# Performance work log

Hardware: AMD Instinct MI355X
Metric: run time of the kernel (lower is better)

The kernel has to match this reference:

```python
import jax, jax.numpy as jnp
import numpy as np

N = 1024          # number of graph nodes
HIDDEN = 128
NUM_HEADS = 8
HEAD_DIM = HIDDEN // NUM_HEADS
E = 16384         # number of edges (avg degree 16)


def _linear_params(key, fin, fout):
    kw, _ = jax.random.split(key)
    W = jax.random.normal(kw, (fin, fout), jnp.float32) / np.sqrt(fin).astype(np.float32)
    b = jnp.zeros((fout,), jnp.float32)
    return W, b


def setup_inputs() -> dict:
    key = jax.random.key(0)
    ks = jax.random.split(key, 12)
    h_prev = jax.random.normal(ks[0], (N, HIDDEN), jnp.float32)
    h_pred = jax.random.normal(ks[1], (N, HIDDEN), jnp.float32)
    adj_rows = jax.random.randint(ks[2], (E,), 0, N, jnp.int32)
    adj_cols = jax.random.randint(ks[3], (E,), 0, N, jnp.int32)
    Wq, bq = _linear_params(ks[4], HIDDEN, HIDDEN)
    Wk, bk = _linear_params(ks[5], HIDDEN, HIDDEN)
    Wv, bv = _linear_params(ks[6], HIDDEN, HIDDEN)
    Wo, bo = _linear_params(ks[7], HIDDEN, HIDDEN)
    gW1, gb1 = _linear_params(ks[8], 2 * HIDDEN, HIDDEN)   # gate MLP layer 1 (silu)
    gW2, gb2 = _linear_params(ks[9], HIDDEN, HIDDEN)       # gate MLP layer 2
    mW1, mb1 = _linear_params(ks[10], 2 * HIDDEN, HIDDEN)  # mixer MLP layer 1 (relu)
    mW2, mb2 = _linear_params(ks[11], HIDDEN, HIDDEN)      # mixer MLP layer 2
    return dict(h_prev=h_prev, h_pred=h_pred, adj_rows=adj_rows, adj_cols=adj_cols,
                Wq=Wq, bq=bq, Wk=Wk, bk=bk, Wv=Wv, bv=bv, Wo=Wo, bo=bo,
                gW1=gW1, gb1=gb1, gW2=gW2, gb2=gb2,
                mW1=mW1, mb1=mb1, mW2=mW2, mb2=mb2)


def reference(h_prev, h_pred, adj_rows, adj_cols,
              Wq, bq, Wk, bk, Wv, bv, Wo, bo,
              gW1, gb1, gW2, gb2, mW1, mb1, mW2, mb2):
    n = h_prev.shape[0]
    # projections, reshaped (n, head_dim, num_heads) exactly as in the source
    q = (h_pred @ Wq + bq).reshape(n, HEAD_DIM, NUM_HEADS)
    k = (h_prev @ Wk + bk).reshape(n, HEAD_DIM, NUM_HEADS)
    v = (h_pred @ Wv + bv).reshape(n, HEAD_DIM, NUM_HEADS)
    # source scales by sqrt(k.shape[-1]) == sqrt(num_heads)
    q = q / jnp.sqrt(jnp.asarray(NUM_HEADS, q.dtype))
    # 'TNH,SNH->TNS': contracts over the num_heads axis -> [n, head_dim, n]
    scores = jnp.einsum('tnh,snh->tns', q, k)
    # bcoo_dot_general(adj, scores, (([1],[0]),([],[]))) == adj @ scores over node axis
    # (duplicate edges accumulate, matching BCOO semantics)
    A = jnp.zeros((n, n), scores.dtype).at[adj_rows, adj_cols].add(jnp.asarray(1.0, scores.dtype))
    attn = jnp.einsum('ts,snd->tnd', A, scores)   # [n, head_dim, n]
    attn = jax.nn.softmax(attn, axis=-1)
    # 'TNS,BNH->BNH': reduce attn over (T,S), broadcast onto v over head_dim axis
    y = jnp.einsum('TNS,BNH->BNH', attn, v)       # [n, head_dim, num_heads]
    out = y.reshape(n, HIDDEN) @ Wo + bo
    # gate MLP (2 layers, silu hidden act, no norm) then sigmoid
    cat = jnp.concatenate([h_pred, h_prev], axis=-1)
    gate = jax.nn.sigmoid(jax.nn.silu(cat @ gW1 + gb1) @ gW2 + gb2)
    out = gate * out
    h_corr = h_prev + out
    # mixer MLP (2 layers, relu hidden act, no norm), residual
    cat2 = jnp.concatenate([h_corr, h_prev], axis=-1)
    mixed = h_corr + (jax.nn.relu(cat2 @ mW1 + mb1) @ mW2 + mb2)
    return mixed
```

## Files before the change

kernel.cpp:

```cpp
#include <hip/hip_runtime.h>


#define HH 128
#define NROWS 1024
#define ROWS 4
#define NT 512
#define NG 16

#define WS_WV  0
#define WS_WO  8192
#define WS_GW1 16384
#define WS_GW2 32768
#define WS_MW1 40960
#define WS_MW2 57344

__device__ __forceinline__ unsigned int f2bf16(float f) {
    union { float f; unsigned int i; } x; x.f = f;
    unsigned int lsb = (x.i >> 16) & 1u;
    return (x.i + 0x7FFFu + lsb) >> 16;
}

__global__ __launch_bounds__(256) void convert_weights(
    const float* __restrict__ Wv,  const float* __restrict__ Wo,
    const float* __restrict__ gW1, const float* __restrict__ gW2,
    const float* __restrict__ mW1, const float* __restrict__ mW2,
    unsigned int* __restrict__ dst)
{
    const int b = blockIdx.x;
    const float* src; unsigned int* d; int lb;
    if      (b < 32)  { src = Wv;  d = dst + WS_WV;  lb = b; }
    else if (b < 64)  { src = Wo;  d = dst + WS_WO;  lb = b - 32; }
    else if (b < 128) { src = gW1; d = dst + WS_GW1; lb = b - 64; }
    else if (b < 160) { src = gW2; d = dst + WS_GW2; lb = b - 128; }
    else if (b < 224) { src = mW1; d = dst + WS_MW1; lb = b - 160; }
    else              { src = mW2; d = dst + WS_MW2; lb = b - 224; }
    const int e  = lb * 256 + threadIdx.x;
    const int k2 = e >> 7, j = e & 127;
    const unsigned int lo = f2bf16(src[(2 * k2) * HH + j]);
    const unsigned int hi = f2bf16(src[(2 * k2 + 1) * HH + j]);
    d[e] = lo | (hi << 16);
}

__device__ __forceinline__ void fma4(float4& a, float s, const float4& w) {
    a.x += s * w.x; a.y += s * w.y; a.z += s * w.z; a.w += s * w.w;
}
__device__ __forceinline__ float4 bflo4(uint4 q) {
    return make_float4(__uint_as_float(q.x << 16), __uint_as_float(q.y << 16),
                       __uint_as_float(q.z << 16), __uint_as_float(q.w << 16));
}
__device__ __forceinline__ float4 bfhi4(uint4 q) {
    return make_float4(__uint_as_float(q.x & 0xffff0000u), __uint_as_float(q.y & 0xffff0000u),
                       __uint_as_float(q.z & 0xffff0000u), __uint_as_float(q.w & 0xffff0000u));
}

__global__ __launch_bounds__(NT) void temporal_attn_fused(
    const float* __restrict__ h_prev,
    const float* __restrict__ h_pred,
    const unsigned int* __restrict__ wbf,
    const float* __restrict__ bv,  const float* __restrict__ bo,
    const float* __restrict__ gb1, const float* __restrict__ gb2,
    const float* __restrict__ mb1, const float* __restrict__ mb2,
    float* __restrict__ out)
{
    __shared__ __align__(16) float sPred[ROWS][HH];
    __shared__ __align__(16) float sPrev[ROWS][HH];
    __shared__ __align__(16) float sBuf[ROWS][HH];
    __shared__ __align__(16) float sCorr[ROWS][HH];
    __shared__ __align__(16) float sAtt[ROWS][HH];
    __shared__ float4 part4[NG][ROWS][HH / 4];

    const int tid = threadIdx.x;
    const int jq  = tid & 31;
    const int cg  = ((tid >> 5) + blockIdx.x) & 15;
    const int rr  = tid >> 7;
    const int jj  = tid & (HH - 1);
    const int r0  = blockIdx.x * ROWS;

    sPred[rr][jj] = h_pred[(r0 + rr) * HH + jj];
    sPrev[rr][jj] = h_prev[(r0 + rr) * HH + jj];
    const float rbv  = bv[jj],  rbo  = bo[jj];
    const float rgb1 = gb1[jj], rgb2 = gb2[jj];
    const float rmb1 = mb1[jj], rmb2 = mb2[jj];
    __syncthreads();

    const float* pf = (const float*)part4;
    const int cbase = rr * HH + jj;

    uint4 wa[8], wb[8];
    float4 acc[ROWS];

    #define LWB(dst, off, wsoff, rp) { \
        const uint4* B4 = (const uint4*)(wbf + (wsoff)); \
        _Pragma("unroll") for (int i = 0; i < 4; ++i) \
            dst[(off) + i] = B4[((rp) + 4 * cg + i) * 32 + jq]; }

    #define ZACC() { _Pragma("unroll") for (int r = 0; r < ROWS; ++r) \
        acc[r] = make_float4(0.f, 0.f, 0.f, 0.f); }

    #define FMAB(S, wp, woff) { \
        _Pragma("unroll") for (int i = 0; i < 4; ++i) { \
            float4 wl = bflo4(wp[(woff) + i]); \
            float4 wh = bfhi4(wp[(woff) + i]); \
            _Pragma("unroll") for (int r = 0; r < ROWS; ++r) { \
                fma4(acc[r], S[r][8 * cg + 2 * i],     wl); \
                fma4(acc[r], S[r][8 * cg + 2 * i + 1], wh); } } }

    #define PSTORE() { \
        _Pragma("unroll") for (int r = 0; r < ROWS; ++r) part4[cg][r][jq] = acc[r]; \
        __syncthreads(); }

    #define COMBINE(dotvar) \
        float dotvar = 0.f; \
        _Pragma("unroll") for (int g = 0; g < NG; ++g) dotvar += pf[g * (ROWS * HH) + cbase];

    LWB(wa, 0, WS_WV, 0);
    LWB(wb, 0, WS_WO, 0);
    ZACC(); FMAB(sPred, wa, 0);
    LWB(wa, 0, WS_GW1, 0);
    LWB(wa, 4, WS_GW1, 64);
    PSTORE();
    { COMBINE(dot); sBuf[rr][jj] = 1024.f * (dot + rbv); }
    __syncthreads();

    ZACC(); FMAB(sBuf, wb, 0);
    LWB(wb, 0, WS_GW2, 0);
    PSTORE();
    { COMBINE(dot); sAtt[rr][jj] = dot + rbo; }
    __syncthreads();

    ZACC(); FMAB(sPred, wa, 0); FMAB(sPrev, wa, 4);
    LWB(wa, 0, WS_MW1, 0);
    LWB(wa, 4, WS_MW1, 64);
    PSTORE();
    { COMBINE(dot);
      float x = dot + rgb1;
      sBuf[rr][jj] = x / (1.f + __expf(-x)); }
    __syncthreads();

    ZACC(); FMAB(sBuf, wb, 0);
    LWB(wb, 0, WS_MW2, 0);
    PSTORE();
    { COMBINE(dot);
      float gate = 1.f / (1.f + __expf(-(dot + rgb2)));
      sCorr[rr][jj] = sPrev[rr][jj] + gate * sAtt[rr][jj]; }
    __syncthreads();

    ZACC(); FMAB(sCorr, wa, 0); FMAB(sPrev, wa, 4);
    PSTORE();
    { COMBINE(dot); sBuf[rr][jj] = fmaxf(dot + rmb1, 0.f); }
    __syncthreads();

    ZACC(); FMAB(sBuf, wb, 0);
    PSTORE();
    { COMBINE(dot); out[(r0 + rr) * HH + jj] = sCorr[rr][jj] + dot + rmb2; }
}

extern "C" void kernel_launch(void* const* d_in, const int* in_sizes, int n_in,
                              void* d_out, int out_size, void* d_ws, size_t ws_size,
                              hipStream_t stream) {
    const float* h_prev = (const float*)d_in[0];
    const float* h_pred = (const float*)d_in[1];
    const float* Wv  = (const float*)d_in[8];
    const float* bv  = (const float*)d_in[9];
    const float* Wo  = (const float*)d_in[10];
    const float* bo  = (const float*)d_in[11];
    const float* gW1 = (const float*)d_in[12];
    const float* gb1 = (const float*)d_in[13];
    const float* gW2 = (const float*)d_in[14];
    const float* gb2 = (const float*)d_in[15];
    const float* mW1 = (const float*)d_in[16];
    const float* mb1 = (const float*)d_in[17];
    const float* mW2 = (const float*)d_in[18];
    const float* mb2 = (const float*)d_in[19];
    float* out = (float*)d_out;
    unsigned int* wbf = (unsigned int*)d_ws;

    hipLaunchKernelGGL(convert_weights, dim3(256), dim3(256), 0, stream,
                       Wv, Wo, gW1, gW2, mW1, mW2, wbf);

    hipLaunchKernelGGL(temporal_attn_fused, dim3(NROWS / ROWS), dim3(NT), 0, stream,
                       h_prev, h_pred, wbf, bv, bo, gb1, gb2, mb1, mb2, out);
}
```

Measured before the change: 99.70 us.

## Drop bf16 weight conversion kernel, read fp32 weights directly, process 8 rows per block

Removes the separate weight-conversion launch and reads the fp32 weights directly in the fused kernel, which also removes the bf16 unpacking. Each block now handles 8 rows instead of 4, halving the grid to 128 blocks so each weight load is reused across more rows. Shared-memory activations are read as float4 vectors. The cost is twice the weight bytes per block, higher register pressure (16+8 float4 weight registers plus 8 accumulators), and fewer blocks to fill the GPU.

After: 100.4 us. About the same (+0.7%).

```diff
diff --git a/kernel.cpp b/kernel.cpp
--- a/kernel.cpp
+++ b/kernel.cpp
@@ -3,63 +3,23 @@
 
 #define HH 128
 #define NROWS 1024
-#define ROWS 4
+#define ROWS 8
 #define NT 512
 #define NG 16
 
-#define WS_WV  0
-#define WS_WO  8192
-#define WS_GW1 16384
-#define WS_GW2 32768
-#define WS_MW1 40960
-#define WS_MW2 57344
-
-__device__ __forceinline__ unsigned int f2bf16(float f) {
-    union { float f; unsigned int i; } x; x.f = f;
-    unsigned int lsb = (x.i >> 16) & 1u;
-    return (x.i + 0x7FFFu + lsb) >> 16;
-}
-
-__global__ __launch_bounds__(256) void convert_weights(
-    const float* __restrict__ Wv,  const float* __restrict__ Wo,
-    const float* __restrict__ gW1, const float* __restrict__ gW2,
-    const float* __restrict__ mW1, const float* __restrict__ mW2,
-    unsigned int* __restrict__ dst)
-{
-    const int b = blockIdx.x;
-    const float* src; unsigned int* d; int lb;
-    if      (b < 32)  { src = Wv;  d = dst + WS_WV;  lb = b; }
-    else if (b < 64)  { src = Wo;  d = dst + WS_WO;  lb = b - 32; }
-    else if (b < 128) { src = gW1; d = dst + WS_GW1; lb = b - 64; }
-    else if (b < 160) { src = gW2; d = dst + WS_GW2; lb = b - 128; }
-    else if (b < 224) { src = mW1; d = dst + WS_MW1; lb = b - 160; }
-    else              { src = mW2; d = dst + WS_MW2; lb = b - 224; }
-    const int e  = lb * 256 + threadIdx.x;
-    const int k2 = e >> 7, j = e & 127;
-    const unsigned int lo = f2bf16(src[(2 * k2) * HH + j]);
-    const unsigned int hi = f2bf16(src[(2 * k2 + 1) * HH + j]);
-    d[e] = lo | (hi << 16);
-}
-
 __device__ __forceinline__ void fma4(float4& a, float s, const float4& w) {
     a.x += s * w.x; a.y += s * w.y; a.z += s * w.z; a.w += s * w.w;
-}
-__device__ __forceinline__ float4 bflo4(uint4 q) {
-    return make_float4(__uint_as_float(q.x << 16), __uint_as_float(q.y << 16),
-                       __uint_as_float(q.z << 16), __uint_as_float(q.w << 16));
-}
-__device__ __forceinline__ float4 bfhi4(uint4 q) {
-    return make_float4(__uint_as_float(q.x & 0xffff0000u), __uint_as_float(q.y & 0xffff0000u),
-                       __uint_as_float(q.z & 0xffff0000u), __uint_as_float(q.w & 0xffff0000u));
 }
 
 __global__ __launch_bounds__(NT) void temporal_attn_fused(
     const float* __restrict__ h_prev,
     const float* __restrict__ h_pred,
-    const unsigned int* __restrict__ wbf,
-    const float* __restrict__ bv,  const float* __restrict__ bo,
-    const float* __restrict__ gb1, const float* __restrict__ gb2,
-    const float* __restrict__ mb1, const float* __restrict__ mb2,
+    const float* __restrict__ Wv,  const float* __restrict__ bv,
+    const float* __restrict__ Wo,  const float* __restrict__ bo,
+    const float* __restrict__ gW1, const float* __restrict__ gb1,
+    const float* __restrict__ gW2, const float* __restrict__ gb2,
+    const float* __restrict__ mW1, const float* __restrict__ mb1,
+    const float* __restrict__ mW2, const float* __restrict__ mb2,
     float* __restrict__ out)
 {
     __shared__ __align__(16) float sPred[ROWS][HH];
@@ -76,83 +36,104 @@
     const int jj  = tid & (HH - 1);
     const int r0  = blockIdx.x * ROWS;
 
-    sPred[rr][jj] = h_pred[(r0 + rr) * HH + jj];
-    sPrev[rr][jj] = h_prev[(r0 + rr) * HH + jj];
+    sPred[rr][jj]     = h_pred[(r0 + rr) * HH + jj];
+    sPred[rr + 4][jj] = h_pred[(r0 + rr + 4) * HH + jj];
+    sPrev[rr][jj]     = h_prev[(r0 + rr) * HH + jj];
+    sPrev[rr + 4][jj] = h_prev[(r0 + rr + 4) * HH + jj];
     const float rbv  = bv[jj],  rbo  = bo[jj];
     const float rgb1 = gb1[jj], rgb2 = gb2[jj];
     const float rmb1 = mb1[jj], rmb2 = mb2[jj];
     __syncthreads();
 
     const float* pf = (const float*)part4;
-    const int cbase = rr * HH + jj;
+    const int cb0 = rr * HH + jj;
+    const int cb1 = (rr + 4) * HH + jj;
 
-    uint4 wa[8], wb[8];
+    float4 wa[16], wb[8];
     float4 acc[ROWS];
 
-    #define LWB(dst, off, wsoff, rp) { \
-        const uint4* B4 = (const uint4*)(wbf + (wsoff)); \
-        _Pragma("unroll") for (int i = 0; i < 4; ++i) \
-            dst[(off) + i] = B4[((rp) + 4 * cg + i) * 32 + jq]; }
+    #define LWF(dst, off, W, rp) { \
+        const float4* B4 = (const float4*)(W); \
+        _Pragma("unroll") for (int i = 0; i < 8; ++i) \
+            dst[(off) + i] = B4[((rp) + 8 * cg + i) * 32 + jq]; }
 
     #define ZACC() { _Pragma("unroll") for (int r = 0; r < ROWS; ++r) \
         acc[r] = make_float4(0.f, 0.f, 0.f, 0.f); }
 
     #define FMAB(S, wp, woff) { \
-        _Pragma("unroll") for (int i = 0; i < 4; ++i) { \
-            float4 wl = bflo4(wp[(woff) + i]); \
-            float4 wh = bfhi4(wp[(woff) + i]); \
-            _Pragma("unroll") for (int r = 0; r < ROWS; ++r) { \
-                fma4(acc[r], S[r][8 * cg + 2 * i],     wl); \
-                fma4(acc[r], S[r][8 * cg + 2 * i + 1], wh); } } }
+        _Pragma("unroll") for (int r = 0; r < ROWS; ++r) { \
+            const float4 s0 = *(const float4*)&S[r][8 * cg]; \
+            const float4 s1 = *(const float4*)&S[r][8 * cg + 4]; \
+            fma4(acc[r], s0.x, wp[(woff) + 0]); \
+            fma4(acc[r], s0.y, wp[(woff) + 1]); \
+            fma4(acc[r], s0.z, wp[(woff) + 2]); \
+            fma4(acc[r], s0.w, wp[(woff) + 3]); \
+            fma4(acc[r], s1.x, wp[(woff) + 4]); \
+            fma4(acc[r], s1.y, wp[(woff) + 5]); \
+            fma4(acc[r], s1.z, wp[(woff) + 6]); \
+            fma4(acc[r], s1.w, wp[(woff) + 7]); } }
 
     #define PSTORE() { \
         _Pragma("unroll") for (int r = 0; r < ROWS; ++r) part4[cg][r][jq] = acc[r]; \
         __syncthreads(); }
 
-    #define COMBINE(dotvar) \
-        float dotvar = 0.f; \
-        _Pragma("unroll") for (int g = 0; g < NG; ++g) dotvar += pf[g * (ROWS * HH) + cbase];
+    #define COMBINE2(d0, d1) \
+        float d0 = 0.f, d1 = 0.f; \
+        _Pragma("unroll") for (int g = 0; g < NG; ++g) { \
+            d0 += pf[g * (ROWS * HH) + cb0]; \
+            d1 += pf[g * (ROWS * HH) + cb1]; }
 
-    LWB(wa, 0, WS_WV, 0);
-    LWB(wb, 0, WS_WO, 0);
+    LWF(wa, 0, Wv, 0);
+    LWF(wb, 0, Wo, 0);
     ZACC(); FMAB(sPred, wa, 0);
-    LWB(wa, 0, WS_GW1, 0);
-    LWB(wa, 4, WS_GW1, 64);
+    LWF(wa, 0, gW1, 0);
+    LWF(wa, 8, gW1, 128);
     PSTORE();
-    { COMBINE(dot); sBuf[rr][jj] = 1024.f * (dot + rbv); }
+    { COMBINE2(d0, d1);
+      sBuf[rr][jj]     = 1024.f * (d0 + rbv);
+      sBuf[rr + 4][jj] = 1024.f * (d1 + rbv); }
     __syncthreads();
 
     ZACC(); FMAB(sBuf, wb, 0);
-    LWB(wb, 0, WS_GW2, 0);
+    LWF(wb, 0, gW2, 0);
     PSTORE();
-    { COMBINE(dot); sAtt[rr][jj] = dot + rbo; }
+    { COMBINE2(d0, d1);
+      sAtt[rr][jj]     = d0 + rbo;
+      sAtt[rr + 4][jj] = d1 + rbo; }
     __syncthreads();
 
-    ZACC(); FMAB(sPred, wa, 0); FMAB(sPrev, wa, 4);
-    LWB(wa, 0, WS_MW1, 0);
-    LWB(wa, 4, WS_MW1, 64);
+    ZACC(); FMAB(sPred, wa, 0); FMAB(sPrev, wa, 8);
+    LWF(wa, 0, mW1, 0);
+    LWF(wa, 8, mW1, 128);
     PSTORE();
-    { COMBINE(dot);
-      float x = dot + rgb1;
-      sBuf[rr][jj] = x / (1.f + __expf(-x)); }
+    { COMBINE2(d0, d1);
+      float x0 = d0 + rgb1, x1 = d1 + rgb1;
+      sBuf[rr][jj]     = x0 / (1.f + __expf(-x0));
+      sBuf[rr + 4][jj] = x1 / (1.f + __expf(-x1)); }
     __syncthreads();
 
     ZACC(); FMAB(sBuf, wb, 0);
-    LWB(wb, 0, WS_MW2, 0);
+    LWF(wb, 0, mW2, 0);
     PSTORE();
-    { COMBINE(dot);
-      float gate = 1.f / (1.f + __expf(-(dot + rgb2)));
-      sCorr[rr][jj] = sPrev[rr][jj] + gate * sAtt[rr][jj]; }
+    { COMBINE2(d0, d1);
+      float g0 = 1.f / (1.f + __expf(-(d0 + rgb2)));
+      float g1 = 1.f / (1.f + __expf(-(d1 + rgb2)));
+      sCorr[rr][jj]     = sPrev[rr][jj]     + g0 * sAtt[rr][jj];
+      sCorr[rr + 4][jj] = sPrev[rr + 4][jj] + g1 * sAtt[rr + 4][jj]; }
     __syncthreads();
 
-    ZACC(); FMAB(sCorr, wa, 0); FMAB(sPrev, wa, 4);
+    ZACC(); FMAB(sCorr, wa, 0); FMAB(sPrev, wa, 8);
     PSTORE();
-    { COMBINE(dot); sBuf[rr][jj] = fmaxf(dot + rmb1, 0.f); }
+    { COMBINE2(d0, d1);
+      sBuf[rr][jj]     = fmaxf(d0 + rmb1, 0.f);
+      sBuf[rr + 4][jj] = fmaxf(d1 + rmb1, 0.f); }
     __syncthreads();
 
     ZACC(); FMAB(sBuf, wb, 0);
     PSTORE();
-    { COMBINE(dot); out[(r0 + rr) * HH + jj] = sCorr[rr][jj] + dot + rmb2; }
+    { COMBINE2(d0, d1);
+      out[(r0 + rr) * HH + jj]     = sCorr[rr][jj]     + d0 + rmb2;
+      out[(r0 + rr + 4) * HH + jj] = sCorr[rr + 4][jj] + d1 + rmb2; }
 }
 
 extern "C" void kernel_launch(void* const* d_in, const int* in_sizes, int n_in,
@@ -173,11 +154,9 @@
     const float* mW2 = (const float*)d_in[18];
     const float* mb2 = (const float*)d_in[19];
     float* out = (float*)d_out;
-    unsigned int* wbf = (unsigned int*)d_ws;
-
-    hipLaunchKernelGGL(convert_weights, dim3(256), dim3(256), 0, stream,
-                       Wv, Wo, gW1, gW2, mW1, mW2, wbf);
+    (void)d_ws; (void)ws_size;
 
     hipLaunchKernelGGL(temporal_attn_fused, dim3(NROWS / ROWS), dim3(NT), 0, stream,
-                       h_prev, h_pred, wbf, bv, bo, gb1, gb2, mb1, mb2, out);
+                       h_prev, h_pred, Wv, bv, Wo, bo, gW1, gb1, gW2, gb2,
+                       mW1, mb1, mW2, mb2, out);
 }
```
